# Optimization experiments

Measured on AMD Instinct MI355X. Metric: run time of the kernel, lower is better.

The kernel has to match this reference:

```python
import jax, jax.numpy as jnp
import numpy as np

EMBED_DIM = 768
NUM_HEAD = 12
HEAD_DIM = 64
SCALE = 1.0 / np.sqrt(HEAD_DIM)


def setup_inputs() -> dict:
    key = jax.random.key(0)
    k1, k2, k3, k4 = jax.random.split(key, 4)
    B, T = 2, 2048
    x = jax.random.normal(k1, (B, T, EMBED_DIM), dtype=jnp.float32)
    # nn.Linear(embed_dim, 3*embed_dim, bias=True): weight [3E, E], bias [3E]
    w_qkv = jax.random.normal(k2, (3 * EMBED_DIM, EMBED_DIM), dtype=jnp.float32) * (1.0 / np.sqrt(EMBED_DIM))
    b_qkv = jax.random.normal(k3, (3 * EMBED_DIM,), dtype=jnp.float32) * 0.02
    # nn.Linear(embed_dim, embed_dim, bias=False): weight [E, E]
    w_final = jax.random.normal(k4, (EMBED_DIM, EMBED_DIM), dtype=jnp.float32) * (1.0 / np.sqrt(EMBED_DIM))
    return {"x": x, "w_qkv": w_qkv, "b_qkv": b_qkv, "w_final": w_final}


def reference(x, w_qkv, b_qkv, w_final):
    B, T, E = x.shape
    # qkv projection: x @ W^T + b  -> [B, T, 3E]
    qkv = jnp.einsum('bte,fe->btf', x, w_qkv) + b_qkv
    q, k, v = jnp.split(qkv, 3, axis=-1)

    def heads(t):  # [B, T, E] -> [B, H, T, D]
        return t.reshape(B, T, NUM_HEAD, HEAD_DIM).transpose(0, 2, 1, 3)

    q, k, v = heads(q), heads(k), heads(v)
    # scores [B, H, T, T]
    scores = jnp.einsum('bhtd,bhsd->bhts', q, k) * SCALE
    causal = jnp.tril(jnp.ones((T, T), dtype=bool))
    scores = jnp.where(causal, scores, -jnp.inf)
    attn = jax.nn.softmax(scores, axis=-1)  # dropout off (eval mode)
    out = jnp.einsum('bhts,bhsd->bhtd', attn, v)  # [B, H, T, D]
    out = out.transpose(0, 2, 1, 3).reshape(B, T, NUM_HEAD * HEAD_DIM)
    return jnp.einsum('bte,fe->btf', out, w_final)
```

## Files before the change

### kernel.cpp

```cpp
#include <hip/hip_runtime.h>
#include <cstdint>

typedef _Float16 f16x8 __attribute__((ext_vector_type(8)));
typedef _Float16 f16x4 __attribute__((ext_vector_type(4)));
typedef float    f32x4 __attribute__((ext_vector_type(4)));

static constexpr int TB = 2;
static constexpr int TT = 2048;
static constexpr int TE = 768;
static constexpr int TH = 12;
static constexpr int TD = 64;
static constexpr int TM = TB * TT;
static constexpr int TK = TE;
static constexpr int NQKV = 3 * TE;

#define SCALE_LOG2E 0.18033688011112042f

__device__ __forceinline__ void gload16(const void* g, void* lds) {
  __builtin_amdgcn_global_load_lds(
      (__attribute__((address_space(1))) void*)(uintptr_t)g,
      (__attribute__((address_space(3))) void*)(uint32_t)(uintptr_t)lds, 16, 0, 0);
}

__global__ void cvt3(const float* __restrict__ x, const float* __restrict__ wq,
                     const float* __restrict__ wf, _Float16* __restrict__ xh,
                     _Float16* __restrict__ wqh, _Float16* __restrict__ wfh) {
  const int NX = TM * TK / 4, NW = NQKV * TK / 4;
  int i = blockIdx.x * 256 + threadIdx.x;
  const float4* src; _Float16* dst; int j;
  if (i < NX)            { src = (const float4*)x;  dst = xh;  j = i; }
  else if (i < NX + NW)  { src = (const float4*)wq; dst = wqh; j = i - NX; }
  else                   { src = (const float4*)wf; dst = wfh; j = i - NX - NW; }
  float4 v = src[j];
  f16x4 o = {(_Float16)v.x, (_Float16)v.y, (_Float16)v.z, (_Float16)v.w};
  *(f16x4*)&dst[(size_t)j * 4] = o;
}

template <int EPI, int NXT>
__global__ __launch_bounds__(512)
void gemm_nt(const _Float16* __restrict__ A, const _Float16* __restrict__ Bw,
             const float* __restrict__ bias,
             _Float16* __restrict__ qb, _Float16* __restrict__ kb,
             _Float16* __restrict__ vtb, float* __restrict__ outp) {
  __shared__ _Float16 As[2][128 * 64];
  __shared__ _Float16 Bs[2][128 * 64];
  const int tid = threadIdx.x;
  const int w = tid >> 6, lane = tid & 63;
  const int lr = lane & 15, lk = lane >> 4;

  const int id = blockIdx.x;
  const int xcd = id & 7, j = id >> 3;
  const int m0 = (xcd * 4 + j / NXT) * 128;
  const int n0 = (j % NXT) * 128;
  const int wr = w >> 2, wc = w & 3;

  f32x4 acc[4][2] = {};
  const char* Ab = (const char*)(A + (size_t)m0 * TK);
  const char* Bb = (const char*)(Bw + (size_t)n0 * TK);
  const char* Tb = (w < 4) ? Ab : Bb;

  auto stage = [&](int k0, int buf) {
    char* Ls = (char*)((w < 4) ? As[buf] : Bs[buf]);
#pragma unroll
    for (int c = 0; c < 4; ++c) {
      int g = (w & 3) * 4 + c;
      int o = g * 1024 + lane * 16;
      int row = o >> 7, ch = (o >> 4) & 7;
      gload16(Tb + (size_t)row * (TK * 2) + k0 * 2 + ((ch ^ (row & 7)) << 4),
              Ls + g * 1024);
    }
  };

  constexpr int NS = TK / 64;
  stage(0, 0);
  for (int ks = 0; ks < NS; ++ks) {
    const int cur = ks & 1;
    if (ks + 1 < NS) {
      stage((ks + 1) * 64, cur ^ 1);
      asm volatile("s_waitcnt vmcnt(4)" ::: "memory");
    } else {
      asm volatile("s_waitcnt vmcnt(0)" ::: "memory");
    }
    __builtin_amdgcn_s_barrier();

#pragma unroll
    for (int kc = 0; kc < 2; ++kc) {
      f16x8 af[4], bf[2];
#pragma unroll
      for (int mi = 0; mi < 4; ++mi) {
        int row = wr * 64 + mi * 16 + lr;
        af[mi] =
            *(const f16x8*)&As[cur][row * 64 + (((kc * 4 + lk) ^ (row & 7)) << 3)];
      }
#pragma unroll
      for (int ni = 0; ni < 2; ++ni) {
        int row = wc * 32 + ni * 16 + lr;
        bf[ni] =
            *(const f16x8*)&Bs[cur][row * 64 + (((kc * 4 + lk) ^ (row & 7)) << 3)];
      }
#pragma unroll
      for (int mi = 0; mi < 4; ++mi)
#pragma unroll
        for (int ni = 0; ni < 2; ++ni)
          acc[mi][ni] = __builtin_amdgcn_mfma_f32_16x16x32_f16(af[mi], bf[ni],
                                                               acc[mi][ni], 0, 0, 0);
    }
    __builtin_amdgcn_s_barrier();
  }

#pragma unroll
  for (int mi = 0; mi < 4; ++mi) {
#pragma unroll
    for (int ni = 0; ni < 2; ++ni) {
      const int col = n0 + wc * 32 + ni * 16 + lr;
#pragma unroll
      for (int r = 0; r < 4; ++r) {
        const int row = m0 + wr * 64 + mi * 16 + lk * 4 + r;
        float v = acc[mi][ni][r];
        if (EPI == 0) {
          v += bias[col];
          const int which = (col >= 2 * TE) ? 2 : (col >= TE ? 1 : 0);
          const int e = col - which * TE;
          const int h = e >> 6, d = e & 63;
          const int b = row >> 11, t = row & (TT - 1);
          const size_t hb = (size_t)(b * TH + h);
          if (which == 0)
            qb[(hb * TT + t) * TD + d] = (_Float16)(v * SCALE_LOG2E);
          else if (which == 1)
            kb[(hb * TT + t) * TD + d] = (_Float16)v;
          else {
            const int u = t & 63;
            const int up = (u & 0x23) | ((u & 0x0C) << 1) | ((u & 0x10) >> 2);
            const int tp = (t & ~63) | up;
            vtb[(hb * TD + d) * TT + tp] = (_Float16)v;
          }
        } else {
          outp[(size_t)row * TE + col] = v;
        }
      }
    }
  }
}

__global__ __launch_bounds__(256)
void attn_kernel(const _Float16* __restrict__ qbuf, const _Float16* __restrict__ kbuf,
                 const _Float16* __restrict__ vtbuf, _Float16* __restrict__ ob) {
  __shared__ _Float16 Ks[2][64 * 64], Vs[2][64 * 64];
  const int tid = threadIdx.x, w = tid >> 6, lane = tid & 63;
  const int lr = lane & 15, lk = lane >> 4;

  const int id = blockIdx.x;
  const int bh = id % 24;
  const int qt = 31 - id / 24;
  const int t0 = qt * 64;

  const size_t hoff = (size_t)bh * (TT * TD);
  const _Float16* q = qbuf + hoff;
  const _Float16* k = kbuf + hoff;
  const _Float16* vt = vtbuf + hoff;
  const int rb = w * 16;

  f16x8 qf[2];
#pragma unroll
  for (int kc = 0; kc < 2; ++kc)
    qf[kc] = *(const f16x8*)&q[(size_t)(t0 + rb + lr) * TD + kc * 32 + lk * 8];

  f32x4 of[4] = {};
  float mrun = -1e30f, lrun = 0.f;

  const int nt = qt + 1;

  auto stage = [&](int st, int buf) {
    const int s0 = st * 64;
#pragma unroll
    for (int c = 0; c < 2; ++c) {
      int o = (w * 2 + c) * 1024 + lane * 16;
      int row = o >> 7, ch = (o >> 4) & 7;
      gload16((const char*)(k + (size_t)s0 * TD) + (size_t)row * 128 +
                  ((ch ^ (row & 7)) << 4),
              (char*)Ks[buf] + (w * 2 + c) * 1024);
      gload16((const char*)(vt + s0) + (size_t)row * (TT * 2) +
                  ((ch ^ (row & 7)) << 4),
              (char*)Vs[buf] + (w * 2 + c) * 1024);
    }
  };

  stage(0, 0);
  for (int st = 0; st < nt; ++st) {
    const int cur = st & 1;
    const int s0 = st * 64;
    if (st + 1 < nt) {
      stage(st + 1, cur ^ 1);
      asm volatile("s_waitcnt vmcnt(4)" ::: "memory");
    } else {
      asm volatile("s_waitcnt vmcnt(0)" ::: "memory");
    }
    __builtin_amdgcn_s_barrier();

    f32x4 sa[4] = {};
    __builtin_amdgcn_s_setprio(1);
#pragma unroll
    for (int kc = 0; kc < 2; ++kc) {
#pragma unroll
      for (int ni = 0; ni < 4; ++ni) {
        int row = ni * 16 + lr;
        f16x8 kf =
            *(const f16x8*)&Ks[cur][row * 64 + (((kc * 4 + lk) ^ (row & 7)) << 3)];
        sa[ni] = __builtin_amdgcn_mfma_f32_16x16x32_f16(kf, qf[kc], sa[ni], 0, 0, 0);
      }
    }
    __builtin_amdgcn_s_setprio(0);

    if (st == nt - 1) {
#pragma unroll
      for (int ni = 0; ni < 4; ++ni)
#pragma unroll
        for (int r = 0; r < 4; ++r)
          if (s0 + ni * 16 + lk * 4 + r > t0 + rb + lr) sa[ni][r] = -1e30f;
    }

    float mx;
    {
      float m0_ = fmaxf(fmaxf(sa[0][0], sa[0][1]), fmaxf(sa[0][2], sa[0][3]));
      float m1_ = fmaxf(fmaxf(sa[1][0], sa[1][1]), fmaxf(sa[1][2], sa[1][3]));
      float m2_ = fmaxf(fmaxf(sa[2][0], sa[2][1]), fmaxf(sa[2][2], sa[2][3]));
      float m3_ = fmaxf(fmaxf(sa[3][0], sa[3][1]), fmaxf(sa[3][2], sa[3][3]));
      mx = fmaxf(fmaxf(m0_, m1_), fmaxf(m2_, m3_));
      mx = fmaxf(mx, __shfl_xor(mx, 16));
      mx = fmaxf(mx, __shfl_xor(mx, 32));
    }

    if (__any(mx > mrun + 8.0f)) {
      float mn = fmaxf(mrun, mx);
      float al = __builtin_amdgcn_exp2f(mrun - mn);
      mrun = mn;
      lrun *= al;
      float al4[4];
#pragma unroll
      for (int r = 0; r < 4; ++r) al4[r] = __shfl(al, lk * 4 + r);
#pragma unroll
      for (int nd = 0; nd < 4; ++nd)
#pragma unroll
        for (int r = 0; r < 4; ++r) of[nd][r] *= al4[r];
    }

    f16x8 pa[2];
    float rs;
    {
      float rn[4];
#pragma unroll
      for (int ni = 0; ni < 4; ++ni) {
        float p0 = __builtin_amdgcn_exp2f(sa[ni][0] - mrun);
        float p1 = __builtin_amdgcn_exp2f(sa[ni][1] - mrun);
        float p2 = __builtin_amdgcn_exp2f(sa[ni][2] - mrun);
        float p3 = __builtin_amdgcn_exp2f(sa[ni][3] - mrun);
        rn[ni] = (p0 + p1) + (p2 + p3);
        pa[ni >> 1][(ni & 1) * 4 + 0] = (_Float16)p0;
        pa[ni >> 1][(ni & 1) * 4 + 1] = (_Float16)p1;
        pa[ni >> 1][(ni & 1) * 4 + 2] = (_Float16)p2;
        pa[ni >> 1][(ni & 1) * 4 + 3] = (_Float16)p3;
      }
      rs = (rn[0] + rn[1]) + (rn[2] + rn[3]);
      rs += __shfl_xor(rs, 16);
      rs += __shfl_xor(rs, 32);
    }
    lrun += rs;

    __builtin_amdgcn_s_setprio(1);
#pragma unroll
    for (int kc = 0; kc < 2; ++kc) {
#pragma unroll
      for (int nd = 0; nd < 4; ++nd) {
        int row = nd * 16 + lr;
        f16x8 vv =
            *(const f16x8*)&Vs[cur][row * 64 + (((kc * 4 + lk) ^ (row & 7)) << 3)];
        of[nd] = __builtin_amdgcn_mfma_f32_16x16x32_f16(pa[kc], vv, of[nd], 0, 0, 0);
      }
    }
    __builtin_amdgcn_s_setprio(0);
    __builtin_amdgcn_s_barrier();
  }

  float linv[4];
#pragma unroll
  for (int r = 0; r < 4; ++r) linv[r] = __shfl(lrun, lk * 4 + r);
  const int b = bh / TH, h = bh - b * TH;
#pragma unroll
  for (int nd = 0; nd < 4; ++nd) {
#pragma unroll
    for (int r = 0; r < 4; ++r) {
      int tg = t0 + rb + lk * 4 + r;
      int d = nd * 16 + lr;
      ob[(size_t)(b * TT + tg) * TE + h * TD + d] = (_Float16)(of[nd][r] / linv[r]);
    }
  }
}

extern "C" void kernel_launch(void* const* d_in, const int* in_sizes, int n_in,
                              void* d_out, int out_size, void* d_ws, size_t ws_size,
                              hipStream_t stream) {
  const float* x    = (const float*)d_in[0];
  const float* wqkv = (const float*)d_in[1];
  const float* bqkv = (const float*)d_in[2];
  const float* wfin = (const float*)d_in[3];
  float* out = (float*)d_out;

  _Float16* xh  = (_Float16*)d_ws;
  _Float16* wqh = xh + (size_t)TM * TK;
  _Float16* wfh = wqh + (size_t)NQKV * TK;
  _Float16* qb  = wfh + (size_t)TE * TE;
  _Float16* kb  = qb + (size_t)TM * TE;
  _Float16* vtb = kb + (size_t)TM * TE;
  _Float16* ob  = vtb + (size_t)TM * TE;

  cvt3<<<5376, 256, 0, stream>>>(x, wqkv, wfin, xh, wqh, wfh);
  gemm_nt<0, NQKV / 128><<<(NQKV / 128) * (TM / 128), 512, 0, stream>>>(
      xh, wqh, bqkv, qb, kb, vtb, nullptr);
  attn_kernel<<<dim3(TT / 64 * TB * TH), 256, 0, stream>>>(qb, kb, vtb, ob);
  gemm_nt<1, TE / 128><<<(TE / 128) * (TM / 128), 512, 0, stream>>>(
      ob, wfh, nullptr, nullptr, nullptr, nullptr, out);
}
```

Baseline: 99.54 us.

## Load K/V fragments directly from global in MFMA layout, drop LDS staging

The QKV epilogue now writes K and V^T in a pre-tiled layout that matches the per-lane MFMA fragment order. The attention kernel can then load K and V fragments straight from global memory into registers. This removes the LDS double buffer and the block barriers, and K is prefetched two tiles ahead in register sets that alternate. Each of the four waves now reads the same K/V tiles separately from global/L2 instead of sharing them through LDS, which raises global traffic and register pressure.

```diff
diff --git a/kernel.cpp b/kernel.cpp
--- a/kernel.cpp
+++ b/kernel.cpp
@@ -124,15 +124,19 @@
           const int h = e >> 6, d = e & 63;
           const int b = row >> 11, t = row & (TT - 1);
           const size_t hb = (size_t)(b * TH + h);
-          if (which == 0)
+          if (which == 0) {
             qb[(hb * TT + t) * TD + d] = (_Float16)(v * SCALE_LOG2E);
-          else if (which == 1)
-            kb[(hb * TT + t) * TD + d] = (_Float16)v;
-          else {
-            const int u = t & 63;
-            const int up = (u & 0x23) | ((u & 0x0C) << 1) | ((u & 0x10) >> 2);
-            const int tp = (t & ~63) | up;
-            vtb[(hb * TD + d) * TT + tp] = (_Float16)v;
+          } else if (which == 1) {
+            kb[((((hb * 128 + (t >> 4)) * 8 + (d >> 3)) * 16 + (t & 15)) * 8) +
+               (d & 7)] = (_Float16)v;
+          } else {
+            const int kc = (t >> 5) & 1, hi = (t >> 4) & 1;
+            const int lkv = (t >> 2) & 3, m = t & 3;
+            vtb[((((((hb * 32 + (t >> 6)) * 4 + (d >> 4)) * 2 + kc) * 4 + lkv) *
+                      16 +
+                  (d & 15)) *
+                 8) +
+                (hi * 4 + m)] = (_Float16)v;
           }
         } else {
           outp[(size_t)row * TE + col] = v;
@@ -145,7 +149,6 @@
 __global__ __launch_bounds__(256)
 void attn_kernel(const _Float16* __restrict__ qbuf, const _Float16* __restrict__ kbuf,
                  const _Float16* __restrict__ vtbuf, _Float16* __restrict__ ob) {
-  __shared__ _Float16 Ks[2][64 * 64], Vs[2][64 * 64];
   const int tid = threadIdx.x, w = tid >> 6, lane = tid & 63;
   const int lr = lane & 15, lk = lane >> 4;
 
@@ -153,70 +156,73 @@
   const int bh = id % 24;
   const int qt = 31 - id / 24;
   const int t0 = qt * 64;
-
-  const size_t hoff = (size_t)bh * (TT * TD);
-  const _Float16* q = qbuf + hoff;
-  const _Float16* k = kbuf + hoff;
-  const _Float16* vt = vtbuf + hoff;
-  const int rb = w * 16;
+  const int nt = qt + 1, ntm1 = qt;
+
+  const _Float16* q = qbuf + (size_t)bh * (TT * TD);
+  const char* kbase =
+      (const char*)(kbuf + (size_t)bh * (TT * TD)) + lk * 256 + lr * 16;
+  const char* vbase =
+      (const char*)(vtbuf + (size_t)bh * (TT * TD)) + lk * 256 + lr * 16;
 
   f16x8 qf[2];
 #pragma unroll
   for (int kc = 0; kc < 2; ++kc)
-    qf[kc] = *(const f16x8*)&q[(size_t)(t0 + rb + lr) * TD + kc * 32 + lk * 8];
+    qf[kc] = *(const f16x8*)&q[(size_t)(t0 + w * 16 + lr) * TD + kc * 32 + lk * 8];
 
   f32x4 of[4] = {};
   float mrun = -1e30f, lrun = 0.f;
 
-  const int nt = qt + 1;
-
-  auto stage = [&](int st, int buf) {
-    const int s0 = st * 64;
-#pragma unroll
-    for (int c = 0; c < 2; ++c) {
-      int o = (w * 2 + c) * 1024 + lane * 16;
-      int row = o >> 7, ch = (o >> 4) & 7;
-      gload16((const char*)(k + (size_t)s0 * TD) + (size_t)row * 128 +
-                  ((ch ^ (row & 7)) << 4),
-              (char*)Ks[buf] + (w * 2 + c) * 1024);
-      gload16((const char*)(vt + s0) + (size_t)row * (TT * 2) +
-                  ((ch ^ (row & 7)) << 4),
-              (char*)Vs[buf] + (w * 2 + c) * 1024);
-    }
-  };
-
-  stage(0, 0);
-  for (int st = 0; st < nt; ++st) {
-    const int cur = st & 1;
-    const int s0 = st * 64;
-    if (st + 1 < nt) {
-      stage(st + 1, cur ^ 1);
-      asm volatile("s_waitcnt vmcnt(4)" ::: "memory");
-    } else {
-      asm volatile("s_waitcnt vmcnt(0)" ::: "memory");
-    }
-    __builtin_amdgcn_s_barrier();
+  f16x8 kfA[2][4], kfB[2][4], vf[2][4];
+
+#pragma unroll
+  for (int kc = 0; kc < 2; ++kc)
+#pragma unroll
+    for (int ni = 0; ni < 4; ++ni)
+      kfA[kc][ni] = *(const f16x8*)(kbase + ni * 2048 + kc * 1024);
+  {
+    const char* k1 = kbase + (size_t)(nt > 1 ? 1 : 0) * 8192;
+#pragma unroll
+    for (int kc = 0; kc < 2; ++kc)
+#pragma unroll
+      for (int ni = 0; ni < 4; ++ni)
+        kfB[kc][ni] = *(const f16x8*)(k1 + ni * 2048 + kc * 1024);
+  }
+
+  auto phase = [&](f16x8 (&kf)[2][4], int st) {
+    const char* vt = vbase + (size_t)st * 8192;
+#pragma unroll
+    for (int kc = 0; kc < 2; ++kc)
+#pragma unroll
+      for (int nd = 0; nd < 4; ++nd)
+        vf[kc][nd] = *(const f16x8*)(vt + nd * 2048 + kc * 1024);
 
     f32x4 sa[4] = {};
     __builtin_amdgcn_s_setprio(1);
 #pragma unroll
-    for (int kc = 0; kc < 2; ++kc) {
-#pragma unroll
-      for (int ni = 0; ni < 4; ++ni) {
-        int row = ni * 16 + lr;
-        f16x8 kf =
-            *(const f16x8*)&Ks[cur][row * 64 + (((kc * 4 + lk) ^ (row & 7)) << 3)];
-        sa[ni] = __builtin_amdgcn_mfma_f32_16x16x32_f16(kf, qf[kc], sa[ni], 0, 0, 0);
-      }
-    }
+    for (int kc = 0; kc < 2; ++kc)
+#pragma unroll
+      for (int ni = 0; ni < 4; ++ni)
+        sa[ni] =
+            __builtin_amdgcn_mfma_f32_16x16x32_f16(kf[kc][ni], qf[kc], sa[ni], 0, 0, 0);
     __builtin_amdgcn_s_setprio(0);
 
-    if (st == nt - 1) {
+    {
+      const int stp = (st + 2 <= ntm1) ? st + 2 : ntm1;
+      const char* kt = kbase + (size_t)stp * 8192;
+#pragma unroll
+      for (int kc = 0; kc < 2; ++kc)
+#pragma unroll
+        for (int ni = 0; ni < 4; ++ni)
+          kf[kc][ni] = *(const f16x8*)(kt + ni * 2048 + kc * 1024);
+    }
+
+    if (st == ntm1) {
+      const int s0 = st * 64;
 #pragma unroll
       for (int ni = 0; ni < 4; ++ni)
 #pragma unroll
         for (int r = 0; r < 4; ++r)
-          if (s0 + ni * 16 + lk * 4 + r > t0 + rb + lr) sa[ni][r] = -1e30f;
+          if (s0 + ni * 16 + lk * 4 + r > t0 + w * 16 + lr) sa[ni][r] = -1e30f;
     }
 
     float mx;
@@ -268,18 +274,21 @@
 
     __builtin_amdgcn_s_setprio(1);
 #pragma unroll
-    for (int kc = 0; kc < 2; ++kc) {
-#pragma unroll
-      for (int nd = 0; nd < 4; ++nd) {
-        int row = nd * 16 + lr;
-        f16x8 vv =
-            *(const f16x8*)&Vs[cur][row * 64 + (((kc * 4 + lk) ^ (row & 7)) << 3)];
-        of[nd] = __builtin_amdgcn_mfma_f32_16x16x32_f16(pa[kc], vv, of[nd], 0, 0, 0);
-      }
-    }
+    for (int kc = 0; kc < 2; ++kc)
+#pragma unroll
+      for (int nd = 0; nd < 4; ++nd)
+        of[nd] =
+            __builtin_amdgcn_mfma_f32_16x16x32_f16(pa[kc], vf[kc][nd], of[nd], 0, 0, 0);
     __builtin_amdgcn_s_setprio(0);
-    __builtin_amdgcn_s_barrier();
-  }
+  };
+
+  int st = 0;
+  while (st + 1 < nt) {
+    phase(kfA, st);
+    phase(kfB, st + 1);
+    st += 2;
+  }
+  if (st < nt) phase(kfA, st);
 
   float linv[4];
 #pragma unroll
@@ -289,7 +298,7 @@
   for (int nd = 0; nd < 4; ++nd) {
 #pragma unroll
     for (int r = 0; r < 4; ++r) {
-      int tg = t0 + rb + lk * 4 + r;
+      int tg = t0 + w * 16 + lk * 4 + r;
       int d = nd * 16 + lr;
       ob[(size_t)(b * TT + tg) * TE + h * TD + d] = (_Float16)(of[nd][r] / linv[r]);
     }
```

Result: faster. 86.71 us (-12.9%).
